# Optimization experiments

Measured on AMD Instinct MI355X. Metric: run time of the kernel, lower is better.

The kernel has to match this reference:

```python
import jax, jax.numpy as jnp
import numpy as np

BATCH, LENGTH, IN, STATE, OUT = 8, 4096, 512, 256, 512


def setup_inputs() -> dict:
    key = jax.random.key(0)
    k1, k2, k3, k4, k5 = jax.random.split(key, 5)
    u = jax.random.normal(k1, (BATCH, LENGTH, IN), dtype=jnp.float32)
    x0 = jax.random.normal(k2, (BATCH, STATE), dtype=jnp.float32)
    A = 0.9999 * (2.0 * jax.random.uniform(k3, (STATE,), dtype=jnp.float32) - 1.0)
    B = jax.random.normal(k4, (IN, STATE), dtype=jnp.float32) / (STATE + IN) ** 0.5
    C = jax.random.normal(k5, (STATE, OUT), dtype=jnp.float32) / STATE ** 0.5
    return {"u": u, "x0": x0, "A": A, "B": B, "C": C}


def reference(u, x0, A, B, C):
    L = u.shape[1]
    # A_powers[t, n] = A[n] ** t, shape [L, state]
    A_powers = jnp.power(A[None, :], jnp.arange(L, dtype=u.dtype)[:, None])
    uB = u @ B  # [batch, L, state]
    # FFT convolution; inputs are real so rfft/irfft gives same result as
    # real(ifft(fft*fft)) in the original.
    T = 2 ** int(np.ceil(np.log2(2 * L - 1)))
    Af = jnp.fft.rfft(A_powers, n=T, axis=0)  # [T/2+1, state]
    Uf = jnp.fft.rfft(uB, n=T, axis=1)        # [batch, T/2+1, state]
    x = jnp.fft.irfft(Af[None, :, :] * Uf, n=T, axis=1)[:, :L]  # [batch, L, state]
    # initial-state contribution: A * A_powers * x0
    x = x + A[None, None, :] * A_powers[None, :, :] * x0[:, None, :]
    y = x @ C  # [batch, L, out]
    return (y, x[:, -1])
```

## Files before the change

### kernel.cpp

```cpp
#include <hip/hip_runtime.h>

#define BATCH   8
#define LENGTH  4096
#define IN_DIM  512
#define STATE   256
#define OUT_DIM 512
#define NC      256
#define LC      16

typedef __attribute__((ext_vector_type(8))) short bf16x8;
typedef __attribute__((ext_vector_type(4))) float f32x4;
typedef __attribute__((ext_vector_type(4))) unsigned short u16x4;

union FragU { bf16x8 v; unsigned u[4]; };

__device__ __forceinline__ unsigned short bf16_rne(float v) {
    unsigned u = __builtin_bit_cast(unsigned, v);
    unsigned r = (u + 0x7FFFu + ((u >> 16) & 1u)) >> 16;
    return (unsigned short)r;
}
__device__ __forceinline__ float bf16_f(unsigned short h) {
    unsigned u = ((unsigned)h) << 16;
    return __builtin_bit_cast(float, u);
}

__global__ __launch_bounds__(256) void split_weights(
    const float* __restrict__ B, const float* __restrict__ C,
    unsigned short* __restrict__ Bhi, unsigned short* __restrict__ Blo,
    unsigned short* __restrict__ Chi, unsigned short* __restrict__ Clo)
{
    int id = blockIdx.x * 256 + threadIdx.x;
    if (id < IN_DIM * STATE) {
        int k = id & (IN_DIM - 1), n = id >> 9;
        float v = B[(size_t)k * STATE + n];
        unsigned short h = bf16_rne(v);
        Bhi[id] = h;
        Blo[id] = bf16_rne(v - bf16_f(h));
    } else {
        int id2 = id - IN_DIM * STATE;
        int k = id2 & (STATE - 1), n = id2 >> 8;
        float v = C[(size_t)k * OUT_DIM + n];
        unsigned short h = bf16_rne(v);
        Chi[id2] = h;
        Clo[id2] = bf16_rne(v - bf16_f(h));
    }
}

__global__ __launch_bounds__(512, 4) void gemm_dbuf(
    const float* __restrict__ Af, const unsigned short* __restrict__ Bthi,
    const unsigned short* __restrict__ Btlo, float* __restrict__ Cc,
    const float* __restrict__ Av, float* __restrict__ carry,
    int N_, int K)
{
    __shared__ unsigned short lds[2 * 16384];

    const int tid  = threadIdx.x;
    const int wave = tid >> 6;
    const int lane = tid & 63;
    const int n0 = blockIdx.x * 128;
    const int m0 = blockIdx.y * 128;

    const char* gp[4];
    int ldsoff[4], gstep[4];
    #pragma unroll
    for (int t = 0; t < 4; ++t) {
        int gi = wave * 4 + t;
        if (gi < 16) {
            int p = gi * 64 + lane;
            int row = p >> 3, s = p & 7;
            int l = s ^ (row & 7);
            gp[t] = (const char*)(Af + (size_t)(m0 + row) * K + l * 4);
            gstep[t] = 32 * 4;
            ldsoff[t] = gi * 512;
        } else {
            int q2 = (gi - 16) >> 3;
            int pi = gi & 7;
            int p = pi * 64 + lane;
            int row = p >> 2, s = p & 3;
            int l = s ^ ((row >> 1) & 3);
            const unsigned short* base = q2 ? Btlo : Bthi;
            gp[t] = (const char*)(base + (size_t)(n0 + row) * K + l * 8);
            gstep[t] = 32 * 2;
            ldsoff[t] = 8192 + q2 * 4096 + pi * 512;
        }
    }

    const int r = lane & 15, q = lane >> 4;
    const int wm = (wave >> 1) * 32, wn = (wave & 1) * 64;

    int aoff[2][2], boff[4];
    #pragma unroll
    for (int i = 0; i < 2; ++i) {
        int row = wm + i * 16 + r;
        #pragma unroll
        for (int h = 0; h < 2; ++h)
            aoff[i][h] = row * 64 + ((2 * q + h) ^ (row & 7)) * 8;
    }
    #pragma unroll
    for (int j = 0; j < 4; ++j) {
        int row = wn + j * 16 + r;
        boff[j] = row * 32 + (q ^ ((row >> 1) & 3)) * 8;
    }

    f32x4 acc[2][4];
    #pragma unroll
    for (int i = 0; i < 2; ++i)
        #pragma unroll
        for (int j = 0; j < 4; ++j)
            acc[i][j] = (f32x4){0.f, 0.f, 0.f, 0.f};

    #pragma unroll
    for (int t = 0; t < 4; ++t) {
        __builtin_amdgcn_global_load_lds(
            (const __attribute__((address_space(1))) unsigned*)(gp[t]),
            (__attribute__((address_space(3))) unsigned*)(&lds[ldsoff[t]]),
            16, 0, 0);
        gp[t] += gstep[t];
    }

    const int nit = K >> 5;
    for (int it = 0; it < nit; ++it) {
        asm volatile("" ::: "memory");
        __builtin_amdgcn_s_barrier();
        asm volatile("" ::: "memory");
        if (it + 1 < nit) {
            const int bb = ((it + 1) & 1) * 16384;
            #pragma unroll
            for (int t = 0; t < 4; ++t) {
                __builtin_amdgcn_global_load_lds(
                    (const __attribute__((address_space(1))) unsigned*)(gp[t]),
                    (__attribute__((address_space(3))) unsigned*)(&lds[bb + ldsoff[t]]),
                    16, 0, 0);
                gp[t] += gstep[t];
            }
            __builtin_amdgcn_s_waitcnt(0x0F74);
        } else {
            __builtin_amdgcn_s_waitcnt(0x0F70);
        }
        asm volatile("" ::: "memory");
        __builtin_amdgcn_s_barrier();
        asm volatile("" ::: "memory");

        const unsigned short* buf = &lds[(it & 1) * 16384];

        FragU ahi[2], alo[2];
        #pragma unroll
        for (int i = 0; i < 2; ++i) {
            #pragma unroll
            for (int h = 0; h < 2; ++h) {
                float4 f = *(const float4*)(buf + aoff[i][h]);
                unsigned bx = __builtin_bit_cast(unsigned, f.x);
                unsigned by = __builtin_bit_cast(unsigned, f.y);
                unsigned bz = __builtin_bit_cast(unsigned, f.z);
                unsigned bw = __builtin_bit_cast(unsigned, f.w);
                ahi[i].u[h * 2]     = __builtin_amdgcn_perm(by, bx, 0x07060302);
                ahi[i].u[h * 2 + 1] = __builtin_amdgcn_perm(bw, bz, 0x07060302);
                float lx = f.x - __builtin_bit_cast(float, bx & 0xFFFF0000u);
                float ly = f.y - __builtin_bit_cast(float, by & 0xFFFF0000u);
                float lz = f.z - __builtin_bit_cast(float, bz & 0xFFFF0000u);
                float lw = f.w - __builtin_bit_cast(float, bw & 0xFFFF0000u);
                alo[i].u[h * 2]     = __builtin_amdgcn_perm(
                    __builtin_bit_cast(unsigned, ly), __builtin_bit_cast(unsigned, lx), 0x07060302);
                alo[i].u[h * 2 + 1] = __builtin_amdgcn_perm(
                    __builtin_bit_cast(unsigned, lw), __builtin_bit_cast(unsigned, lz), 0x07060302);
            }
        }
        FragU bhi[4], blo[4];
        #pragma unroll
        for (int j = 0; j < 4; ++j) {
            bhi[j].v = *(const bf16x8*)(buf +  8192 + boff[j]);
            blo[j].v = *(const bf16x8*)(buf + 12288 + boff[j]);
        }
        #pragma unroll
        for (int i = 0; i < 2; ++i)
            #pragma unroll
            for (int j = 0; j < 4; ++j) {
                acc[i][j] = __builtin_amdgcn_mfma_f32_16x16x32_bf16(ahi[i].v, bhi[j].v, acc[i][j], 0, 0, 0);
                acc[i][j] = __builtin_amdgcn_mfma_f32_16x16x32_bf16(alo[i].v, bhi[j].v, acc[i][j], 0, 0, 0);
                acc[i][j] = __builtin_amdgcn_mfma_f32_16x16x32_bf16(ahi[i].v, blo[j].v, acc[i][j], 0, 0, 0);
            }
    }

    #pragma unroll
    for (int i = 0; i < 2; ++i) {
        #pragma unroll
        for (int reg = 0; reg < 4; ++reg) {
            int mg = m0 + wm + i * 16 + q * 4 + reg;
            float* dst = Cc + (size_t)mg * N_ + n0 + wn + r;
            dst[0]  = acc[i][0][reg];
            dst[16] = acc[i][1][reg];
            dst[32] = acc[i][2][reg];
            dst[48] = acc[i][3][reg];
        }
    }

    {
        const int b  = m0 >> 12;
        const int c0 = ((m0 & 4095) + wm) >> 4;
        #pragma unroll
        for (int j = 0; j < 4; ++j) {
            const int n = n0 + wn + j * 16 + r;
            const float a  = Av[n];
            const float a2 = a * a, a3 = a2 * a, a4 = a2 * a2;
            const float a8 = a4 * a4, a12 = a8 * a4;
            const float base = (q == 0) ? a12 : (q == 1) ? a8 : (q == 2) ? a4 : 1.f;
            #pragma unroll
            for (int i = 0; i < 2; ++i) {
                float partial = base * (a3 * acc[i][j][0] + a2 * acc[i][j][1]
                                      + a  * acc[i][j][2] +      acc[i][j][3]);
                partial += __shfl_xor(partial, 16);
                partial += __shfl_xor(partial, 32);
                if (q == 0)
                    carry[((size_t)b * NC + (c0 + i)) * STATE + n] = partial;
            }
        }
    }
}

__global__ __launch_bounds__(512, 4) void gemm_presplit(
    const unsigned short* __restrict__ Athi, const unsigned short* __restrict__ Atlo,
    const unsigned short* __restrict__ Bthi, const unsigned short* __restrict__ Btlo,
    float* __restrict__ Cc, int N_, int K)
{
    __shared__ unsigned short lds[2 * 16384];

    const int tid  = threadIdx.x;
    const int wave = tid >> 6;
    const int lane = tid & 63;
    const int n0 = blockIdx.x * 128;
    const int m0 = blockIdx.y * 128;

    const char* gp[4];
    int ldsoff[4];
    #pragma unroll
    for (int t = 0; t < 4; ++t) {
        int gi = wave * 4 + t;
        int plane = gi >> 3;
        int pi = gi & 7;
        int p = pi * 64 + lane;
        int row = p >> 2, s = p & 3;
        int l = s ^ ((row >> 1) & 3);
        const unsigned short* base =
            (plane == 0) ? Athi : (plane == 1) ? Atlo : (plane == 2) ? Bthi : Btlo;
        int r0 = (plane < 2) ? m0 : n0;
        gp[t] = (const char*)(base + (size_t)(r0 + row) * K + l * 8);
        ldsoff[t] = plane * 4096 + pi * 512;
    }

    const int r = lane & 15, q = lane >> 4;
    const int wm = (wave >> 2) * 64, wn = (wave & 3) * 32;

    int aoff[4], boff[2];
    #pragma unroll
    for (int i = 0; i < 4; ++i) {
        int row = wm + i * 16 + r;
        aoff[i] = row * 32 + (q ^ ((row >> 1) & 3)) * 8;
    }
    #pragma unroll
    for (int j = 0; j < 2; ++j) {
        int row = wn + j * 16 + r;
        boff[j] = row * 32 + (q ^ ((row >> 1) & 3)) * 8;
    }

    f32x4 acc[4][2];
    #pragma unroll
    for (int i = 0; i < 4; ++i)
        #pragma unroll
        for (int j = 0; j < 2; ++j)
            acc[i][j] = (f32x4){0.f, 0.f, 0.f, 0.f};

    #pragma unroll
    for (int t = 0; t < 4; ++t) {
        __builtin_amdgcn_global_load_lds(
            (const __attribute__((address_space(1))) unsigned*)(gp[t]),
            (__attribute__((address_space(3))) unsigned*)(&lds[ldsoff[t]]),
            16, 0, 0);
        gp[t] += 64;
    }

    const int nit = K >> 5;
    for (int it = 0; it < nit; ++it) {
        asm volatile("" ::: "memory");
        __builtin_amdgcn_s_barrier();
        asm volatile("" ::: "memory");
        if (it + 1 < nit) {
            const int bb = ((it + 1) & 1) * 16384;
            #pragma unroll
            for (int t = 0; t < 4; ++t) {
                __builtin_amdgcn_global_load_lds(
                    (const __attribute__((address_space(1))) unsigned*)(gp[t]),
                    (__attribute__((address_space(3))) unsigned*)(&lds[bb + ldsoff[t]]),
                    16, 0, 0);
                gp[t] += 64;
            }
            __builtin_amdgcn_s_waitcnt(0x0F74);
        } else {
            __builtin_amdgcn_s_waitcnt(0x0F70);
        }
        asm volatile("" ::: "memory");
        __builtin_amdgcn_s_barrier();
        asm volatile("" ::: "memory");

        const unsigned short* buf = &lds[(it & 1) * 16384];

        FragU ahi[4], alo[4];
        #pragma unroll
        for (int i = 0; i < 4; ++i) {
            ahi[i].v = *(const bf16x8*)(buf +        aoff[i]);
            alo[i].v = *(const bf16x8*)(buf + 4096 + aoff[i]);
        }
        FragU bhi[2], blo[2];
        #pragma unroll
        for (int j = 0; j < 2; ++j) {
            bhi[j].v = *(const bf16x8*)(buf +  8192 + boff[j]);
            blo[j].v = *(const bf16x8*)(buf + 12288 + boff[j]);
        }
        #pragma unroll
        for (int i = 0; i < 4; ++i)
            #pragma unroll
            for (int j = 0; j < 2; ++j) {
                acc[i][j] = __builtin_amdgcn_mfma_f32_16x16x32_bf16(ahi[i].v, bhi[j].v, acc[i][j], 0, 0, 0);
                acc[i][j] = __builtin_amdgcn_mfma_f32_16x16x32_bf16(alo[i].v, bhi[j].v, acc[i][j], 0, 0, 0);
                acc[i][j] = __builtin_amdgcn_mfma_f32_16x16x32_bf16(ahi[i].v, blo[j].v, acc[i][j], 0, 0, 0);
            }
    }

    #pragma unroll
    for (int i = 0; i < 4; ++i) {
        #pragma unroll
        for (int reg = 0; reg < 4; ++reg) {
            int mg = m0 + wm + i * 16 + q * 4 + reg;
            float* dst = Cc + (size_t)mg * N_ + n0 + wn + r;
            dst[0]  = acc[i][0][reg];
            dst[16] = acc[i][1][reg];
        }
    }
}

__global__ __launch_bounds__(256) void scan_entries(
    const float* __restrict__ carry, const float* __restrict__ A,
    const float* __restrict__ x0, float* __restrict__ entry)
{
    const int b = blockIdx.x;
    const int n = threadIdx.x;
    const float a = A[n];
    float aL = a;
    #pragma unroll
    for (int k = 0; k < 4; ++k) aL *= aL;

    float s = x0[(size_t)b * STATE + n];
    const float* cr = carry + (size_t)b * NC * STATE + n;
    float* en = entry + (size_t)b * NC * STATE + n;
    #pragma unroll 8
    for (int c = 0; c < NC; ++c) {
        en[(size_t)c * STATE] = s;
        s = fmaf(aL, s, cr[(size_t)c * STATE]);
    }
}

__global__ __launch_bounds__(64) void scan_apply(
    const float* __restrict__ uB, const float* __restrict__ A,
    const float* __restrict__ entry,
    unsigned short* __restrict__ xhi, unsigned short* __restrict__ xlo,
    float* __restrict__ x_last)
{
    const int b = blockIdx.x;
    const int c = blockIdx.y;
    const int t = threadIdx.x;
    const float4 a = *(const float4*)(A + 4 * t);

    const size_t base = ((size_t)b * LENGTH + (size_t)c * LC) * STATE;
    const float4* p = (const float4*)(uB + base) + t;

    float4 v[LC];
    #pragma unroll
    for (int j = 0; j < LC; ++j) v[j] = p[(size_t)j * (STATE / 4)];

    float4 s = *((const float4*)(entry + ((size_t)b * NC + c) * STATE) + t);

    u16x4* qh = (u16x4*)(xhi + base) + t;
    u16x4* ql = (u16x4*)(xlo + base) + t;
    #pragma unroll
    for (int j = 0; j < LC; ++j) {
        s.x = fmaf(a.x, s.x, v[j].x);
        s.y = fmaf(a.y, s.y, v[j].y);
        s.z = fmaf(a.z, s.z, v[j].z);
        s.w = fmaf(a.w, s.w, v[j].w);
        u16x4 hh, ll;
        unsigned ux = __builtin_bit_cast(unsigned, s.x);
        unsigned uy = __builtin_bit_cast(unsigned, s.y);
        unsigned uz = __builtin_bit_cast(unsigned, s.z);
        unsigned uw = __builtin_bit_cast(unsigned, s.w);
        hh[0] = (unsigned short)(ux >> 16);
        hh[1] = (unsigned short)(uy >> 16);
        hh[2] = (unsigned short)(uz >> 16);
        hh[3] = (unsigned short)(uw >> 16);
        float lx = s.x - __builtin_bit_cast(float, ux & 0xFFFF0000u);
        float ly = s.y - __builtin_bit_cast(float, uy & 0xFFFF0000u);
        float lz = s.z - __builtin_bit_cast(float, uz & 0xFFFF0000u);
        float lw = s.w - __builtin_bit_cast(float, uw & 0xFFFF0000u);
        ll[0] = (unsigned short)(__builtin_bit_cast(unsigned, lx) >> 16);
        ll[1] = (unsigned short)(__builtin_bit_cast(unsigned, ly) >> 16);
        ll[2] = (unsigned short)(__builtin_bit_cast(unsigned, lz) >> 16);
        ll[3] = (unsigned short)(__builtin_bit_cast(unsigned, lw) >> 16);
        qh[(size_t)j * (STATE / 4)] = hh;
        ql[(size_t)j * (STATE / 4)] = ll;
    }
    if (c == NC - 1)
        *((float4*)(x_last + (size_t)b * STATE) + t) = s;
}

extern "C" void kernel_launch(void* const* d_in, const int* in_sizes, int n_in,
                              void* d_out, int out_size, void* d_ws, size_t ws_size,
                              hipStream_t stream)
{
    const float* u  = (const float*)d_in[0];
    const float* x0 = (const float*)d_in[1];
    const float* A  = (const float*)d_in[2];
    const float* B  = (const float*)d_in[3];
    const float* C  = (const float*)d_in[4];

    const size_t MB = 1024 * 1024;
    char* ws = (char*)d_ws;

    unsigned short* xhi = (unsigned short*)(ws);
    unsigned short* xlo = (unsigned short*)(ws + 16 * MB);
    float* carry = (float*)(ws + 32 * MB);
    float* entry = (float*)(ws + 34 * MB);
    unsigned short* Bt_hi = (unsigned short*)(ws + 36 * MB);
    unsigned short* Bt_lo = (unsigned short*)(ws + 36 * MB + 256 * 1024);
    unsigned short* Ct_hi = (unsigned short*)(ws + 36 * MB + 512 * 1024);
    unsigned short* Ct_lo = (unsigned short*)(ws + 36 * MB + 768 * 1024);

    float* y      = (float*)d_out;
    float* x_last = y + (size_t)BATCH * LENGTH * OUT_DIM;
    float* uB     = (float*)((char*)d_out + 32 * MB);

    const int M = BATCH * LENGTH;

    split_weights<<<dim3((IN_DIM * STATE + STATE * OUT_DIM) / 256), dim3(256), 0, stream>>>(
        B, C, Bt_hi, Bt_lo, Ct_hi, Ct_lo);

    gemm_dbuf<<<dim3(STATE / 128, M / 128), dim3(512), 0, stream>>>(
        u, Bt_hi, Bt_lo, uB, A, carry, STATE, IN_DIM);

    scan_entries<<<dim3(BATCH), dim3(256), 0, stream>>>(carry, A, x0, entry);
    scan_apply<<<dim3(BATCH, NC), dim3(64), 0, stream>>>(uB, A, entry, xhi, xlo, x_last);

    gemm_presplit<<<dim3(OUT_DIM / 128, M / 128), dim3(512), 0, stream>>>(
        xhi, xlo, Ct_hi, Ct_lo, y, OUT_DIM, STATE);
}
```

Before: 205.8 us.

## Fuse chunk scan apply and bf16 split into the output GEMM prologue

Result: faster. 194.6 us (-5.4%).

```diff
diff --git a/kernel.cpp b/kernel.cpp
--- a/kernel.cpp
+++ b/kernel.cpp
@@ -10,7 +10,6 @@
 
 typedef __attribute__((ext_vector_type(8))) short bf16x8;
 typedef __attribute__((ext_vector_type(4))) float f32x4;
-typedef __attribute__((ext_vector_type(4))) unsigned short u16x4;
 
 union FragU { bf16x8 v; unsigned u[4]; };
 
@@ -217,10 +216,34 @@
     }
 }
 
-__global__ __launch_bounds__(512, 4) void gemm_presplit(
-    const unsigned short* __restrict__ Athi, const unsigned short* __restrict__ Atlo,
-    const unsigned short* __restrict__ Bthi, const unsigned short* __restrict__ Btlo,
-    float* __restrict__ Cc, int N_, int K)
+__global__ __launch_bounds__(256) void scan_entries(
+    const float* __restrict__ carry, const float* __restrict__ A,
+    const float* __restrict__ x0, float* __restrict__ entry,
+    float* __restrict__ x_last)
+{
+    const int b = blockIdx.x;
+    const int n = threadIdx.x;
+    const float a = A[n];
+    float aL = a;
+    #pragma unroll
+    for (int k = 0; k < 4; ++k) aL *= aL;
+
+    float s = x0[(size_t)b * STATE + n];
+    const float* cr = carry + (size_t)b * NC * STATE + n;
+    float* en = entry + (size_t)b * NC * STATE + n;
+    #pragma unroll 16
+    for (int c = 0; c < NC; ++c) {
+        en[(size_t)c * STATE] = s;
+        s = fmaf(aL, s, cr[(size_t)c * STATE]);
+    }
+    x_last[(size_t)b * STATE + n] = s;
+}
+
+__global__ __launch_bounds__(512, 4) void gemm_scan_apply(
+    const float* __restrict__ uB, const unsigned short* __restrict__ Bthi,
+    const unsigned short* __restrict__ Btlo, const float* __restrict__ Av,
+    const float* __restrict__ entry, float* __restrict__ Cc,
+    int N_, int K)
 {
     __shared__ unsigned short lds[2 * 16384];
 
@@ -229,44 +252,59 @@
     const int lane = tid & 63;
     const int n0 = blockIdx.x * 128;
     const int m0 = blockIdx.y * 128;
+    const int bb_ = m0 >> 12;
+    const int c0_ = (m0 & 4095) >> 4;
 
     const char* gp[4];
-    int ldsoff[4];
+    int ldsoff[4], gstep[4];
     #pragma unroll
     for (int t = 0; t < 4; ++t) {
         int gi = wave * 4 + t;
-        int plane = gi >> 3;
-        int pi = gi & 7;
-        int p = pi * 64 + lane;
-        int row = p >> 2, s = p & 3;
-        int l = s ^ ((row >> 1) & 3);
-        const unsigned short* base =
-            (plane == 0) ? Athi : (plane == 1) ? Atlo : (plane == 2) ? Bthi : Btlo;
-        int r0 = (plane < 2) ? m0 : n0;
-        gp[t] = (const char*)(base + (size_t)(r0 + row) * K + l * 8);
-        ldsoff[t] = plane * 4096 + pi * 512;
+        if (gi < 16) {
+            int p = gi * 64 + lane;
+            int row = p >> 3, s = p & 7;
+            int l = s ^ (row & 7);
+            gp[t] = (const char*)(uB + (size_t)(m0 + row) * K + l * 4);
+            gstep[t] = 32 * 4;
+            ldsoff[t] = gi * 512;
+        } else {
+            int q2 = (gi - 16) >> 3;
+            int pi = gi & 7;
+            int p = pi * 64 + lane;
+            int row = p >> 2, s = p & 3;
+            int l = s ^ ((row >> 1) & 3);
+            const unsigned short* base = q2 ? Btlo : Bthi;
+            gp[t] = (const char*)(base + (size_t)(n0 + row) * K + l * 8);
+            gstep[t] = 32 * 2;
+            ldsoff[t] = 8192 + q2 * 4096 + pi * 512;
+        }
     }
 
     const int r = lane & 15, q = lane >> 4;
-    const int wm = (wave >> 2) * 64, wn = (wave & 3) * 32;
-
-    int aoff[4], boff[2];
-    #pragma unroll
-    for (int i = 0; i < 4; ++i) {
+    const int wm = (wave >> 1) * 32, wn = (wave & 1) * 64;
+
+    int aoff[2][2], boff[4];
+    #pragma unroll
+    for (int i = 0; i < 2; ++i) {
         int row = wm + i * 16 + r;
-        aoff[i] = row * 32 + (q ^ ((row >> 1) & 3)) * 8;
-    }
-    #pragma unroll
-    for (int j = 0; j < 2; ++j) {
+        #pragma unroll
+        for (int h = 0; h < 2; ++h)
+            aoff[i][h] = row * 64 + ((2 * q + h) ^ (row & 7)) * 8;
+    }
+    #pragma unroll
+    for (int j = 0; j < 4; ++j) {
         int row = wn + j * 16 + r;
         boff[j] = row * 32 + (q ^ ((row >> 1) & 3)) * 8;
     }
 
-    f32x4 acc[4][2];
-    #pragma unroll
-    for (int i = 0; i < 4; ++i)
-        #pragma unroll
-        for (int j = 0; j < 2; ++j)
+    const int sc = tid >> 5;
+    const int sk = tid & 31;
+
+    f32x4 acc[2][4];
+    #pragma unroll
+    for (int i = 0; i < 2; ++i)
+        #pragma unroll
+        for (int j = 0; j < 4; ++j)
             acc[i][j] = (f32x4){0.f, 0.f, 0.f, 0.f};
 
     #pragma unroll
@@ -275,7 +313,7 @@
             (const __attribute__((address_space(1))) unsigned*)(gp[t]),
             (__attribute__((address_space(3))) unsigned*)(&lds[ldsoff[t]]),
             16, 0, 0);
-        gp[t] += 64;
+        gp[t] += gstep[t];
     }
 
     const int nit = K >> 5;
@@ -291,7 +329,7 @@
                     (const __attribute__((address_space(1))) unsigned*)(gp[t]),
                     (__attribute__((address_space(3))) unsigned*)(&lds[bb + ldsoff[t]]),
                     16, 0, 0);
-                gp[t] += 64;
+                gp[t] += gstep[t];
             }
             __builtin_amdgcn_s_waitcnt(0x0F74);
         } else {
@@ -301,24 +339,58 @@
         __builtin_amdgcn_s_barrier();
         asm volatile("" ::: "memory");
 
-        const unsigned short* buf = &lds[(it & 1) * 16384];
-
-        FragU ahi[4], alo[4];
-        #pragma unroll
-        for (int i = 0; i < 4; ++i) {
-            ahi[i].v = *(const bf16x8*)(buf +        aoff[i]);
-            alo[i].v = *(const bf16x8*)(buf + 4096 + aoff[i]);
-        }
-        FragU bhi[2], blo[2];
-        #pragma unroll
-        for (int j = 0; j < 2; ++j) {
+        unsigned short* bufw = &lds[(it & 1) * 16384];
+        const unsigned short* buf = bufw;
+
+        if (tid < 256) {
+            const int kg = it * 32 + sk;
+            const float a = Av[kg];
+            float s = entry[((size_t)bb_ * NC + (c0_ + sc)) * STATE + kg];
+            #pragma unroll
+            for (int j = 0; j < 16; ++j) {
+                int row = sc * 16 + j;
+                int off = row * 64 + (((sk >> 2) ^ (row & 7)) * 8) + ((sk & 3) * 2);
+                float v = *(const float*)(bufw + off);
+                s = fmaf(a, s, v);
+                *(float*)(bufw + off) = s;
+            }
+        }
+        asm volatile("s_waitcnt lgkmcnt(0)" ::: "memory");
+        __builtin_amdgcn_s_barrier();
+        asm volatile("" ::: "memory");
+
+        FragU ahi[2], alo[2];
+        #pragma unroll
+        for (int i = 0; i < 2; ++i) {
+            #pragma unroll
+            for (int h = 0; h < 2; ++h) {
+                float4 f = *(const float4*)(buf + aoff[i][h]);
+                unsigned bx = __builtin_bit_cast(unsigned, f.x);
+                unsigned by = __builtin_bit_cast(unsigned, f.y);
+                unsigned bz = __builtin_bit_cast(unsigned, f.z);
+                unsigned bw = __builtin_bit_cast(unsigned, f.w);
+                ahi[i].u[h * 2]     = __builtin_amdgcn_perm(by, bx, 0x07060302);
+                ahi[i].u[h * 2 + 1] = __builtin_amdgcn_perm(bw, bz, 0x07060302);
+                float lx = f.x - __builtin_bit_cast(float, bx & 0xFFFF0000u);
+                float ly = f.y - __builtin_bit_cast(float, by & 0xFFFF0000u);
+                float lz = f.z - __builtin_bit_cast(float, bz & 0xFFFF0000u);
+                float lw = f.w - __builtin_bit_cast(float, bw & 0xFFFF0000u);
+                alo[i].u[h * 2]     = __builtin_amdgcn_perm(
+                    __builtin_bit_cast(unsigned, ly), __builtin_bit_cast(unsigned, lx), 0x07060302);
+                alo[i].u[h * 2 + 1] = __builtin_amdgcn_perm(
+                    __builtin_bit_cast(unsigned, lw), __builtin_bit_cast(unsigned, lz), 0x07060302);
+            }
+        }
+        FragU bhi[4], blo[4];
+        #pragma unroll
+        for (int j = 0; j < 4; ++j) {
             bhi[j].v = *(const bf16x8*)(buf +  8192 + boff[j]);
             blo[j].v = *(const bf16x8*)(buf + 12288 + boff[j]);
         }
         #pragma unroll
-        for (int i = 0; i < 4; ++i)
-            #pragma unroll
-            for (int j = 0; j < 2; ++j) {
+        for (int i = 0; i < 2; ++i)
+            #pragma unroll
+            for (int j = 0; j < 4; ++j) {
                 acc[i][j] = __builtin_amdgcn_mfma_f32_16x16x32_bf16(ahi[i].v, bhi[j].v, acc[i][j], 0, 0, 0);
                 acc[i][j] = __builtin_amdgcn_mfma_f32_16x16x32_bf16(alo[i].v, bhi[j].v, acc[i][j], 0, 0, 0);
                 acc[i][j] = __builtin_amdgcn_mfma_f32_16x16x32_bf16(ahi[i].v, blo[j].v, acc[i][j], 0, 0, 0);
@@ -326,88 +398,17 @@
     }
 
     #pragma unroll
-    for (int i = 0; i < 4; ++i) {
+    for (int i = 0; i < 2; ++i) {
         #pragma unroll
         for (int reg = 0; reg < 4; ++reg) {
             int mg = m0 + wm + i * 16 + q * 4 + reg;
             float* dst = Cc + (size_t)mg * N_ + n0 + wn + r;
             dst[0]  = acc[i][0][reg];
             dst[16] = acc[i][1][reg];
-        }
-    }
-}
-
-__global__ __launch_bounds__(256) void scan_entries(
-    const float* __restrict__ carry, const float* __restrict__ A,
-    const float* __restrict__ x0, float* __restrict__ entry)
-{
-    const int b = blockIdx.x;
-    const int n = threadIdx.x;
-    const float a = A[n];
-    float aL = a;
-    #pragma unroll
-    for (int k = 0; k < 4; ++k) aL *= aL;
-
-    float s = x0[(size_t)b * STATE + n];
-    const float* cr = carry + (size_t)b * NC * STATE + n;
-    float* en = entry + (size_t)b * NC * STATE + n;
-    #pragma unroll 8
-    for (int c = 0; c < NC; ++c) {
-        en[(size_t)c * STATE] = s;
-        s = fmaf(aL, s, cr[(size_t)c * STATE]);
-    }
-}
-
-__global__ __launch_bounds__(64) void scan_apply(
-    const float* __restrict__ uB, const float* __restrict__ A,
-    const float* __restrict__ entry,
-    unsigned short* __restrict__ xhi, unsigned short* __restrict__ xlo,
-    float* __restrict__ x_last)
-{
-    const int b = blockIdx.x;
-    const int c = blockIdx.y;
-    const int t = threadIdx.x;
-    const float4 a = *(const float4*)(A + 4 * t);
-
-    const size_t base = ((size_t)b * LENGTH + (size_t)c * LC) * STATE;
-    const float4* p = (const float4*)(uB + base) + t;
-
-    float4 v[LC];
-    #pragma unroll
-    for (int j = 0; j < LC; ++j) v[j] = p[(size_t)j * (STATE / 4)];
-
-    float4 s = *((const float4*)(entry + ((size_t)b * NC + c) * STATE) + t);
-
-    u16x4* qh = (u16x4*)(xhi + base) + t;
-    u16x4* ql = (u16x4*)(xlo + base) + t;
-    #pragma unroll
-    for (int j = 0; j < LC; ++j) {
-        s.x = fmaf(a.x, s.x, v[j].x);
-        s.y = fmaf(a.y, s.y, v[j].y);
-        s.z = fmaf(a.z, s.z, v[j].z);
-        s.w = fmaf(a.w, s.w, v[j].w);
-        u16x4 hh, ll;
-        unsigned ux = __builtin_bit_cast(unsigned, s.x);
-        unsigned uy = __builtin_bit_cast(unsigned, s.y);
-        unsigned uz = __builtin_bit_cast(unsigned, s.z);
-        unsigned uw = __builtin_bit_cast(unsigned, s.w);
-        hh[0] = (unsigned short)(ux >> 16);
-        hh[1] = (unsigned short)(uy >> 16);
-        hh[2] = (unsigned short)(uz >> 16);
-        hh[3] = (unsigned short)(uw >> 16);
-        float lx = s.x - __builtin_bit_cast(float, ux & 0xFFFF0000u);
-        float ly = s.y - __builtin_bit_cast(float, uy & 0xFFFF0000u);
-        float lz = s.z - __builtin_bit_cast(float, uz & 0xFFFF0000u);
-        float lw = s.w - __builtin_bit_cast(float, uw & 0xFFFF0000u);
-        ll[0] = (unsigned short)(__builtin_bit_cast(unsigned, lx) >> 16);
-        ll[1] = (unsigned short)(__builtin_bit_cast(unsigned, ly) >> 16);
-        ll[2] = (unsigned short)(__builtin_bit_cast(unsigned, lz) >> 16);
-        ll[3] = (unsigned short)(__builtin_bit_cast(unsigned, lw) >> 16);
-        qh[(size_t)j * (STATE / 4)] = hh;
-        ql[(size_t)j * (STATE / 4)] = ll;
-    }
-    if (c == NC - 1)
-        *((float4*)(x_last + (size_t)b * STATE) + t) = s;
+            dst[32] = acc[i][2][reg];
+            dst[48] = acc[i][3][reg];
+        }
+    }
 }
 
 extern "C" void kernel_launch(void* const* d_in, const int* in_sizes, int n_in,
@@ -423,8 +424,7 @@
     const size_t MB = 1024 * 1024;
     char* ws = (char*)d_ws;
 
-    unsigned short* xhi = (unsigned short*)(ws);
-    unsigned short* xlo = (unsigned short*)(ws + 16 * MB);
+    float* uB    = (float*)(ws);
     float* carry = (float*)(ws + 32 * MB);
     float* entry = (float*)(ws + 34 * MB);
     unsigned short* Bt_hi = (unsigned short*)(ws + 36 * MB);
@@ -434,7 +434,6 @@
 
     float* y      = (float*)d_out;
     float* x_last = y + (size_t)BATCH * LENGTH * OUT_DIM;
-    float* uB     = (float*)((char*)d_out + 32 * MB);
 
     const int M = BATCH * LENGTH;
 
@@ -444,9 +443,8 @@
     gemm_dbuf<<<dim3(STATE / 128, M / 128), dim3(512), 0, stream>>>(
         u, Bt_hi, Bt_lo, uB, A, carry, STATE, IN_DIM);
 
-    scan_entries<<<dim3(BATCH), dim3(256), 0, stream>>>(carry, A, x0, entry);
-    scan_apply<<<dim3(BATCH, NC), dim3(64), 0, stream>>>(uB, A, entry, xhi, xlo, x_last);
-
-    gemm_presplit<<<dim3(OUT_DIM / 128, M / 128), dim3(512), 0, stream>>>(
-        xhi, xlo, Ct_hi, Ct_lo, y, OUT_DIM, STATE);
-}
+    scan_entries<<<dim3(BATCH), dim3(256), 0, stream>>>(carry, A, x0, entry, x_last);
+
+    gemm_scan_apply<<<dim3(OUT_DIM / 128, M / 128), dim3(512), 0, stream>>>(
+        uB, Ct_hi, Ct_lo, A, entry, y, OUT_DIM, STATE);
+}
```
